# Performance work log

Hardware: AMD Instinct MI355X
Metric: run time of the kernel (lower is better)

## Reference

```python
import jax, jax.numpy as jnp
import numpy as np

K = 5  # hard-coded neighbor count in get_graph_feature


def _graph_feature(x):
    # x: (B, C, N) -> (B, 2C, N, K)
    xt = jnp.swapaxes(x, 1, 2)                      # (B, N, C)
    sq = jnp.sum(xt * xt, axis=-1)                  # (B, N)
    inner = jnp.einsum('bnc,bmc->bnm', xt, xt)      # (B, N, N)
    pdist = 2.0 * inner - sq[:, :, None] - sq[:, None, :]  # -||xi-xj||^2
    idx = jax.lax.top_k(pdist, K)[1]                # (B, N, K) nearest (incl self)
    nbr = jax.vmap(lambda f, i: f[i])(xt, idx)      # (B, N, K, C) gather
    ctr = jnp.broadcast_to(xt[:, :, None, :], nbr.shape)
    feat = jnp.concatenate([nbr, ctr], axis=-1)     # (B, N, K, 2C)
    return jnp.transpose(feat, (0, 3, 1, 2))        # (B, 2C, N, K)


def _conv1x1(w, x):
    # w: (Cout, Cin), x: (B, Cin, N, K)
    return jnp.einsum('oc,bcnk->bonk', w, x)


def setup_inputs() -> dict:
    key = jax.random.key(0)
    ks = jax.random.split(key, 6)
    B, N = 4, 8192
    x = jax.random.normal(ks[0], (B, 3, N), dtype=jnp.float32)

    def xavier(k, cout, cin):
        std = (2.0 / (cin + cout)) ** 0.5
        return std * jax.random.normal(k, (cout, cin), dtype=jnp.float32)

    return {
        'x': x,
        'w1': xavier(ks[1], 64, 6),
        'w2': xavier(ks[2], 64, 64),
        'w3': xavier(ks[3], 128, 64),
        'w4': xavier(ks[4], 256, 128),
        'w5': xavier(ks[5], 512, 512),
    }


def reference(x, w1, w2, w3, w4, w5):
    B, _, N = x.shape
    h = _graph_feature(x)                           # (B, 6, N, K)
    h = jax.nn.relu(_conv1x1(w1, h))
    x1 = jnp.max(h, axis=-1, keepdims=True)         # (B, 64, N, 1)
    h = jax.nn.relu(_conv1x1(w2, h))
    x2 = jnp.max(h, axis=-1, keepdims=True)         # (B, 64, N, 1)
    h = jax.nn.relu(_conv1x1(w3, h))
    x3 = jnp.max(h, axis=-1, keepdims=True)         # (B, 128, N, 1)
    h = jax.nn.relu(_conv1x1(w4, h))
    x4 = jnp.max(h, axis=-1, keepdims=True)         # (B, 256, N, 1)
    cat = jnp.concatenate([x1, x2, x3, x4], axis=1) # (B, 512, N, 1)
    out = jax.nn.relu(_conv1x1(w5, cat))            # (B, 512, N, 1)
    return out.reshape(B, -1, N)
```

## Files before the change

### kernel.cpp

```cpp
#include <hip/hip_runtime.h>
#include <cstdint>

#define BATCH 4
#define NPTS  8192
#define KNN   5
#define CAPQ  176

typedef short bf16x8 __attribute__((ext_vector_type(8)));
typedef float f32x4  __attribute__((ext_vector_type(4)));
#define MFMA16(a, b, c) __builtin_amdgcn_mfma_f32_16x16x32_bf16((a), (b), (c), 0, 0, 0)

__device__ __forceinline__ unsigned short f2bf(float x) {
    unsigned u = __float_as_uint(x);
    unsigned r = u + 0x7fffu + ((u >> 16) & 1u);
    return (unsigned short)(r >> 16);
}
__device__ __forceinline__ float bf2f(unsigned short h) {
    return __uint_as_float(((unsigned)h) << 16);
}
__device__ __forceinline__ void gload16(const void* g, void* l) {
    __builtin_amdgcn_global_load_lds(
        (const __attribute__((address_space(1))) unsigned int*)g,
        (__attribute__((address_space(3))) unsigned int*)l, 16, 0, 0);
}

__global__ __launch_bounds__(256) void wsplit_kernel(
        const float* __restrict__ w3, const float* __restrict__ w4,
        const float* __restrict__ w5, const float* __restrict__ x,
        unsigned short* __restrict__ w3H, unsigned short* __restrict__ w3L,
        unsigned short* __restrict__ w4H, unsigned short* __restrict__ w4L,
        unsigned short* __restrict__ w5H, unsigned short* __restrict__ w5L,
        float* __restrict__ c2) {
    const int i = blockIdx.x * 256 + threadIdx.x;
    if (i >= 303104) {
        const int pt = i - 303104;
        const int b = pt >> 13, n = pt & 8191;
        const float* xb = x + (size_t)b * 3 * NPTS;
        const float cx = xb[n], cy = xb[NPTS + n], cz = xb[2 * NPTS + n];
        c2[pt] = fmaf(cz, cz, fmaf(cy, cy, cx * cx));
        return;
    }
    const float* src; unsigned short *dh, *dl; int off;
    if (i < 8192)       { src = w3; dh = w3H; dl = w3L; off = i; }
    else if (i < 40960) { src = w4; dh = w4H; dl = w4L; off = i - 8192; }
    else                { src = w5; dh = w5H; dl = w5L; off = i - 40960; }
    const float v = src[off];
    const unsigned short hi = f2bf(v);
    dh[off] = hi;
    dl[off] = f2bf(v - bf2f(hi));
}

__global__ __launch_bounds__(1024, 8) void knn_kernel(const float* __restrict__ x,
                                                      const float* __restrict__ c2,
                                                      int* __restrict__ idx_out) {
    __shared__ __align__(16) char sbuf[32768];
    __shared__ __align__(16) char buf2[45056];
    __shared__ float  thrQ[64];
    __shared__ int    qcnt[64];

    float* thrA = (float*)buf2;
    int*   qidx = (int*)buf2;

    const int t = threadIdx.x;
    const int lane = t & 63;
    const int s = t >> 6;
    const int b = blockIdx.x >> 7;
    const int q0 = (blockIdx.x & 127) * 64;
    const int qg = q0 + lane;
    const float* xb = x + (size_t)b * 3 * NPTS;

    float4* stw = ((float4*)sbuf) + s * 128;
    double* qd  = (double*)sbuf;

    const float nqx = -2.0f * xb[qg];
    const float nqy = -2.0f * xb[NPTS + qg];
    const float nqz = -2.0f * xb[2 * NPTS + qg];

    if (t < 64) qcnt[t] = 0;

    const float2* gx = (const float2*)xb;
    const float2* gy = (const float2*)(xb + NPTS);
    const float2* gz = (const float2*)(xb + 2 * NPTS);
    const float2* gc = (const float2*)(c2 + b * NPTS);
    const int f2base = s * 256;

    float s0 = 3e38f, s1 = 3e38f, s2 = 3e38f, s3 = 3e38f, s4 = 3e38f;
    {
        float2 xv = gx[f2base + lane], yv = gy[f2base + lane];
        float2 zv = gz[f2base + lane], cv = gc[f2base + lane];
        for (int ch = 0; ch < 4; ++ch) {
            stw[0 * 64 + lane] = make_float4(xv.x, yv.x, zv.x, cv.x);
            stw[1 * 64 + lane] = make_float4(xv.y, yv.y, zv.y, cv.y);
            if (ch < 3) {
                const int f2 = f2base + (ch + 1) * 64 + lane;
                xv = gx[f2]; yv = gy[f2]; zv = gz[f2]; cv = gc[f2];
            }
            for (int u4 = 0; u4 < 32; ++u4) {
                float4 cd[4];
                #pragma unroll
                for (int j = 0; j < 4; ++j) cd[j] = stw[u4 * 4 + j];
                float d[4];
                #pragma unroll
                for (int j = 0; j < 4; ++j)
                    d[j] = fmaf(cd[j].x, nqx,
                           fmaf(cd[j].y, nqy, fmaf(cd[j].z, nqz, cd[j].w)));
                const float m0 = fminf(d[0], d[1]);
                const float m1 = fminf(d[2], d[3]);
                s4 = __builtin_amdgcn_fmed3f(s3, m0, s4);
                s3 = __builtin_amdgcn_fmed3f(s2, m0, s3);
                s2 = __builtin_amdgcn_fmed3f(s1, m0, s2);
                s1 = __builtin_amdgcn_fmed3f(s0, m0, s1);
                s0 = fminf(s0, m0);
                s4 = __builtin_amdgcn_fmed3f(s3, m1, s4);
                s3 = __builtin_amdgcn_fmed3f(s2, m1, s3);
                s2 = __builtin_amdgcn_fmed3f(s1, m1, s2);
                s1 = __builtin_amdgcn_fmed3f(s0, m1, s1);
                s0 = fminf(s0, m1);
            }
        }
    }
    thrA[s * 64 + lane] = s4;
    __syncthreads();
    if (t < 64) {
        float m = thrA[t];
        #pragma unroll
        for (int ww = 1; ww < 16; ++ww) m = fminf(m, thrA[ww * 64 + t]);
        thrQ[t] = m + 4e-4f;
    }
    __syncthreads();

    const float thrq = thrQ[lane];
    {
        float2 xv = gx[f2base + lane], yv = gy[f2base + lane];
        float2 zv = gz[f2base + lane], cv = gc[f2base + lane];
        for (int ch = 0; ch < 4; ++ch) {
            const int cb = s * 512 + ch * 128;
            stw[0 * 64 + lane] = make_float4(xv.x, yv.x, zv.x, cv.x);
            stw[1 * 64 + lane] = make_float4(xv.y, yv.y, zv.y, cv.y);
            if (ch < 3) {
                const int f2 = f2base + (ch + 1) * 64 + lane;
                xv = gx[f2]; yv = gy[f2]; zv = gz[f2]; cv = gc[f2];
            }
            for (int u4 = 0; u4 < 32; ++u4) {
                float4 cd[4];
                #pragma unroll
                for (int j = 0; j < 4; ++j) cd[j] = stw[u4 * 4 + j];
                float d[4];
                #pragma unroll
                for (int j = 0; j < 4; ++j)
                    d[j] = fmaf(cd[j].x, nqx,
                           fmaf(cd[j].y, nqy, fmaf(cd[j].z, nqz, cd[j].w)));
                const float dmin = fminf(fminf(d[0], d[1]), fminf(d[2], d[3]));
                if (dmin < thrq) {
                    #pragma unroll
                    for (int j = 0; j < 4; ++j) {
                        if (d[j] < thrq) {
                            const int slot = atomicAdd(&qcnt[lane], 1);
                            const int u = u4 * 4 + j;
                            const int gid = cb + 2 * (u & 63) + (u >> 6);
                            if (slot < CAPQ) qidx[lane * CAPQ + slot] = gid;
                        }
                    }
                }
            }
        }
    }

    const int qll = t >> 6;
    const int jt = t & 63;
    for (int ph = 0; ph < 4; ++ph) {
        __syncthreads();
        const int ql = ph * 16 + qll;
        const int cnt = min(qcnt[ql], CAPQ);
        const double Qx = (double)xb[q0 + ql];
        const double Qy = (double)xb[NPTS + q0 + ql];
        const double Qz = (double)xb[2 * NPTS + q0 + ql];
        for (int j = jt; j < cnt; j += 64) {
            const int ci = qidx[ql * CAPQ + j];
            const double ddx = Qx - (double)xb[ci];
            const double ddy = Qy - (double)xb[NPTS + ci];
            const double ddz = Qz - (double)xb[2 * NPTS + ci];
            qd[qll * CAPQ + j] = ddx * ddx + ddy * ddy + ddz * ddz;
        }
        __syncthreads();
        for (int j = jt; j < cnt; j += 64) {
            const double dj = qd[qll * CAPQ + j];
            const int    ij = qidx[ql * CAPQ + j];
            int rank = 0;
            for (int k = 0; k < cnt; ++k) {
                const double dk = qd[qll * CAPQ + k];
                const int    ik = qidx[ql * CAPQ + k];
                rank += (dk < dj) || (dk == dj && ik < ij);
            }
            if (rank < KNN)
                idx_out[((size_t)b * NPTS + q0 + ql) * KNN + rank] = ij;
        }
    }
}

__global__ __launch_bounds__(256) void mlp12_kernel(const float* __restrict__ x,
                                                    const int* __restrict__ idx,
                                                    const float* __restrict__ w1,
                                                    const float* __restrict__ w2,
                                                    unsigned short* __restrict__ h2HL,
                                                    unsigned short* __restrict__ catH,
                                                    unsigned short* __restrict__ catL) {
    __shared__ float w1s[64 * 6];
    __shared__ float w2s[64 * 68];
    __shared__ float fbuf[80][6];
    __shared__ float h1s[80 * 68];
    __shared__ float h2s[80 * 68];
    const int t = threadIdx.x;
    const int pbase = blockIdx.x * 16;

    for (int i = t; i < 384; i += 256) w1s[i] = w1[i];
    for (int i = t; i < 4096; i += 256) {
        int c = i >> 6, q = i & 63;
        w2s[c * 68 + q] = w2[i];
    }
    if (t < 80) {
        const int pt = pbase + t / 5;
        const int b = pt >> 13;
        const int n = pt & 8191;
        const int k = t % 5;
        const int j = idx[(size_t)pt * KNN + k];
        const float* xb = x + (size_t)b * 3 * NPTS;
        fbuf[t][0] = xb[j];
        fbuf[t][1] = xb[NPTS + j];
        fbuf[t][2] = xb[2 * NPTS + j];
        fbuf[t][3] = xb[n];
        fbuf[t][4] = xb[NPTS + n];
        fbuf[t][5] = xb[2 * NPTS + n];
    }
    __syncthreads();

    for (int o = t; o < 5120; o += 256) {
        const int r = o >> 6, c = o & 63;
        float acc = 0.f;
        #pragma unroll
        for (int q = 0; q < 6; ++q) acc = fmaf(w1s[c * 6 + q], fbuf[r][q], acc);
        h1s[r * 68 + c] = fmaxf(acc, 0.f);
    }
    __syncthreads();

    for (int o = t; o < 1024; o += 256) {
        const int p = o >> 6, c = o & 63;
        float m = h1s[(p * 5) * 68 + c];
        #pragma unroll
        for (int k = 1; k < 5; ++k) m = fmaxf(m, h1s[(p * 5 + k) * 68 + c]);
        const unsigned short hi = f2bf(m);
        const size_t co = (size_t)(pbase + p) * 512 + c;
        catH[co] = hi;
        catL[co] = f2bf(m - bf2f(hi));
    }

    for (int tile = t; tile < 320; tile += 256) {
        const int r0 = (tile % 20) * 4;
        const int c0 = (tile / 20) * 4;
        float acc[4][4] = {};
        for (int q = 0; q < 64; q += 4) {
            float4 a[4], w[4];
            #pragma unroll
            for (int i = 0; i < 4; ++i) a[i] = *(const float4*)&h1s[(r0 + i) * 68 + q];
            #pragma unroll
            for (int j = 0; j < 4; ++j) w[j] = *(const float4*)&w2s[(c0 + j) * 68 + q];
            #pragma unroll
            for (int i = 0; i < 4; ++i)
                #pragma unroll
                for (int j = 0; j < 4; ++j) {
                    acc[i][j] = fmaf(a[i].x, w[j].x, acc[i][j]);
                    acc[i][j] = fmaf(a[i].y, w[j].y, acc[i][j]);
                    acc[i][j] = fmaf(a[i].z, w[j].z, acc[i][j]);
                    acc[i][j] = fmaf(a[i].w, w[j].w, acc[i][j]);
                }
        }
        #pragma unroll
        for (int i = 0; i < 4; ++i)
            #pragma unroll
            for (int j = 0; j < 4; ++j)
                h2s[(r0 + i) * 68 + c0 + j] = fmaxf(acc[i][j], 0.f);
    }
    __syncthreads();

    for (int o = t; o < 1024; o += 256) {
        const int p = o >> 6, c = o & 63;
        float m = h2s[(p * 5) * 68 + c];
        #pragma unroll
        for (int k = 1; k < 5; ++k) m = fmaxf(m, h2s[(p * 5 + k) * 68 + c]);
        const unsigned short hi = f2bf(m);
        const size_t co = (size_t)(pbase + p) * 512 + 64 + c;
        catH[co] = hi;
        catL[co] = f2bf(m - bf2f(hi));
    }
    for (int o = t; o < 5120; o += 256) {
        const int r = o >> 6, c = o & 63;
        const float v = h2s[r * 68 + c];
        const unsigned short hi = f2bf(v);
        const size_t rowb = (size_t)(pbase * 5 + r) * 128;
        h2HL[rowb + c]      = hi;
        h2HL[rowb + 64 + c] = f2bf(v - bf2f(hi));
    }
}

__global__ __launch_bounds__(256) void mlp3_kernel(
        const unsigned short* __restrict__ h2HL,
        const unsigned short* __restrict__ w3H, const unsigned short* __restrict__ w3L,
        unsigned short* __restrict__ h3H, unsigned short* __restrict__ h3L,
        unsigned short* __restrict__ catH, unsigned short* __restrict__ catL) {
    __shared__ __align__(16) char smem[59904];
    unsigned short* aH = (unsigned short*)smem;
    unsigned short* aL = aH + 80 * 72;
    unsigned short* bH = (unsigned short*)(smem + 23040);
    unsigned short* bL = (unsigned short*)(smem + 41472);

    const int t = threadIdx.x;
    const int R0 = blockIdx.x * 80;
    const int P0 = blockIdx.x * 16;

    for (int c = t; c < 1280; c += 256) {
        const int row = c >> 4, seg = c & 15;
        const uint4 v = *(const uint4*)(h2HL + (size_t)(R0 + row) * 128 + seg * 8);
        *(uint4*)((seg < 8 ? aH : aL) + row * 72 + (seg & 7) * 8) = v;
    }
    for (int c = t; c < 1024; c += 256) {
        const int row = c >> 3, seg = c & 7;
        *(uint4*)(bH + row * 72 + seg * 8) =
            *(const uint4*)(w3H + row * 64 + seg * 8);
    }
    for (int c = t; c < 1024; c += 256) {
        const int row = c >> 3, seg = c & 7;
        *(uint4*)(bL + row * 72 + seg * 8) =
            *(const uint4*)(w3L + row * 64 + seg * 8);
    }
    __syncthreads();

    const int w = t >> 6, lane = t & 63;
    const int q = lane >> 4, l16 = lane & 15;
    const int n0 = w * 32;

    f32x4 acc[5][2];
    #pragma unroll
    for (int mt = 0; mt < 5; ++mt)
        #pragma unroll
        for (int nt = 0; nt < 2; ++nt)
            acc[mt][nt] = (f32x4){0.f, 0.f, 0.f, 0.f};

    #pragma unroll
    for (int kt = 0; kt < 2; ++kt) {
        const int k0 = kt * 32 + q * 8;
        bf16x8 bh[2], bl[2];
        #pragma unroll
        for (int nt = 0; nt < 2; ++nt) {
            bh[nt] = *(const bf16x8*)(bH + (n0 + nt * 16 + l16) * 72 + k0);
            bl[nt] = *(const bf16x8*)(bL + (n0 + nt * 16 + l16) * 72 + k0);
        }
        #pragma unroll
        for (int mt = 0; mt < 5; ++mt) {
            const bf16x8 ah = *(const bf16x8*)(aH + (mt * 16 + l16) * 72 + k0);
            const bf16x8 al = *(const bf16x8*)(aL + (mt * 16 + l16) * 72 + k0);
            #pragma unroll
            for (int nt = 0; nt < 2; ++nt) {
                acc[mt][nt] = MFMA16(ah, bh[nt], acc[mt][nt]);
                acc[mt][nt] = MFMA16(ah, bl[nt], acc[mt][nt]);
                acc[mt][nt] = MFMA16(al, bh[nt], acc[mt][nt]);
            }
        }
    }

    __syncthreads();
    float* Dbuf = (float*)smem;
    #pragma unroll
    for (int mt = 0; mt < 5; ++mt)
        #pragma unroll
        for (int nt = 0; nt < 2; ++nt)
            #pragma unroll
            for (int r = 0; r < 4; ++r)
                Dbuf[(mt * 16 + q * 4 + r) * 132 + n0 + nt * 16 + l16] =
                    fmaxf(acc[mt][nt][r], 0.f);
    __syncthreads();

    {
        const int col = t & 127;
        const int p0 = (t >> 7) * 8;
        #pragma unroll
        for (int p = 0; p < 8; ++p) {
            const int pp = p0 + p;
            float mx = 0.f;
            #pragma unroll
            for (int k = 0; k < 5; ++k) {
                const int row = pp * 5 + k;
                const float v = Dbuf[row * 132 + col];
                const unsigned short hi = f2bf(v);
                const unsigned short lo = f2bf(v - bf2f(hi));
                const size_t off = (size_t)(R0 + row) * 128 + col;
                h3H[off] = hi;
                h3L[off] = lo;
                mx = fmaxf(mx, bf2f(hi) + bf2f(lo));
            }
            const unsigned short mh = f2bf(mx);
            const size_t co = (size_t)(P0 + pp) * 512 + 128 + col;
            catH[co] = mh;
            catL[co] = f2bf(mx - bf2f(mh));
        }
    }
}

__global__ __launch_bounds__(256) void mlp4_kernel(
        const unsigned short* __restrict__ h3H, const unsigned short* __restrict__ h3L,
        const unsigned short* __restrict__ w4H, const unsigned short* __restrict__ w4L,
        unsigned short* __restrict__ catH, unsigned short* __restrict__ catL) {
    __shared__ __align__(16) char smem[64000];
    unsigned short* aH = (unsigned short*)smem;
    unsigned short* aL = aH + 80 * 136;
    unsigned short* bH = (unsigned short*)(smem + 43520);
    unsigned short* bL = (unsigned short*)(smem + 53760);

    const int t = threadIdx.x;
    const int R0 = blockIdx.x * 80;
    const int P0 = blockIdx.x * 16;
    const int ny = blockIdx.y;

    for (int c = t; c < 1280; c += 256) {
        const int row = c >> 4, seg = c & 15;
        *(uint4*)(aH + row * 136 + seg * 8) =
            *(const uint4*)(h3H + (size_t)(R0 + row) * 128 + seg * 8);
    }
    for (int c = t; c < 1280; c += 256) {
        const int row = c >> 4, seg = c & 15;
        *(uint4*)(aL + row * 136 + seg * 8) =
            *(const uint4*)(h3L + (size_t)(R0 + row) * 128 + seg * 8);
    }

    const int w = t >> 6, lane = t & 63;
    const int q = lane >> 4, l16 = lane & 15;
    const int n0 = w * 32;

    f32x4 acc[5][2];
    #pragma unroll
    for (int mt = 0; mt < 5; ++mt)
        #pragma unroll
        for (int nt = 0; nt < 2; ++nt)
            acc[mt][nt] = (f32x4){0.f, 0.f, 0.f, 0.f};

    for (int ks = 0; ks < 4; ++ks) {
        __syncthreads();
        #pragma unroll
        for (int i = 0; i < 2; ++i) {
            const int c = t + i * 256;
            const int row = c >> 2, seg = c & 3;
            *(uint4*)(bH + row * 40 + seg * 8) =
                *(const uint4*)(w4H + (size_t)(ny * 128 + row) * 128 + ks * 32 + seg * 8);
        }
        #pragma unroll
        for (int i = 0; i < 2; ++i) {
            const int c = t + i * 256;
            const int row = c >> 2, seg = c & 3;
            *(uint4*)(bL + row * 40 + seg * 8) =
                *(const uint4*)(w4L + (size_t)(ny * 128 + row) * 128 + ks * 32 + seg * 8);
        }
        __syncthreads();

        const int k0 = ks * 32 + q * 8;
        const int kb = q * 8;
        bf16x8 bh[2], bl[2];
        #pragma unroll
        for (int nt = 0; nt < 2; ++nt) {
            bh[nt] = *(const bf16x8*)(bH + (n0 + nt * 16 + l16) * 40 + kb);
            bl[nt] = *(const bf16x8*)(bL + (n0 + nt * 16 + l16) * 40 + kb);
        }
        #pragma unroll
        for (int mt = 0; mt < 5; ++mt) {
            const bf16x8 ah = *(const bf16x8*)(aH + (mt * 16 + l16) * 136 + k0);
            const bf16x8 al = *(const bf16x8*)(aL + (mt * 16 + l16) * 136 + k0);
            #pragma unroll
            for (int nt = 0; nt < 2; ++nt) {
                acc[mt][nt] = MFMA16(ah, bh[nt], acc[mt][nt]);
                acc[mt][nt] = MFMA16(ah, bl[nt], acc[mt][nt]);
                acc[mt][nt] = MFMA16(al, bh[nt], acc[mt][nt]);
            }
        }
    }

    __syncthreads();
    float* Dbuf = (float*)smem;
    #pragma unroll
    for (int mt = 0; mt < 5; ++mt)
        #pragma unroll
        for (int nt = 0; nt < 2; ++nt)
            #pragma unroll
            for (int r = 0; r < 4; ++r)
                Dbuf[(mt * 16 + q * 4 + r) * 132 + n0 + nt * 16 + l16] =
                    fmaxf(acc[mt][nt][r], 0.f);
    __syncthreads();

    {
        const int col = t & 127;
        const int p0 = (t >> 7) * 8;
        const int cout = 256 + ny * 128 + col;
        #pragma unroll
        for (int p = 0; p < 8; ++p) {
            const int pp = p0 + p;
            float mx = 0.f;
            #pragma unroll
            for (int k = 0; k < 5; ++k)
                mx = fmaxf(mx, Dbuf[(pp * 5 + k) * 132 + col]);
            const unsigned short mh = f2bf(mx);
            const size_t co = (size_t)(P0 + pp) * 512 + cout;
            catH[co] = mh;
            catL[co] = f2bf(mx - bf2f(mh));
        }
    }
}

__global__ __launch_bounds__(256) void gemm512_kernel(
        const unsigned short* __restrict__ catH, const unsigned short* __restrict__ catL,
        const unsigned short* __restrict__ w5H, const unsigned short* __restrict__ w5L,
        float* __restrict__ out) {
    __shared__ __align__(16) char smem[32768];
    unsigned short* aH = (unsigned short*)smem;
    unsigned short* aL = aH + 128 * 32;
    unsigned short* bH = (unsigned short*)(smem + 16384);
    unsigned short* bL = (unsigned short*)(smem + 24576);

    const int t = threadIdx.x;
    const int m0 = blockIdx.x * 128;
    const int n0blk = blockIdx.y * 128;

    const int w = t >> 6, lane = t & 63;
    const int q = lane >> 4, l16 = lane & 15;
    const int m_off = (w >> 1) * 64;
    const int n_off = (w & 1) * 64;

    const int srow = w * 32 + (lane >> 2);
    const int sseg = lane & 3;
    const size_t ar0 = (size_t)(m0 + srow) * 512 + sseg * 8;
    const size_t ar1 = ar0 + 16 * 512;
    const size_t br0 = (size_t)(n0blk + srow) * 512 + sseg * 8;
    const size_t br1 = br0 + 16 * 512;
    const int ld0 = w * 1024;

    f32x4 acc[4][4];
    #pragma unroll
    for (int mt = 0; mt < 4; ++mt)
        #pragma unroll
        for (int nt = 0; nt < 4; ++nt)
            acc[mt][nt] = (f32x4){0.f, 0.f, 0.f, 0.f};

    for (int kc = 0; kc < 512; kc += 32) {
        __syncthreads();
        gload16(catH + ar0 + kc, aH + ld0);
        gload16(catH + ar1 + kc, aH + ld0 + 512);
        gload16(catL + ar0 + kc, aL + ld0);
        gload16(catL + ar1 + kc, aL + ld0 + 512);
        gload16(w5H + br0 + kc, bH + ld0);
        gload16(w5H + br1 + kc, bH + ld0 + 512);
        gload16(w5L + br0 + kc, bL + ld0);
        gload16(w5L + br1 + kc, bL + ld0 + 512);
        __syncthreads();

        const int k0 = q * 8;
        bf16x8 bh[4], bl[4];
        #pragma unroll
        for (int nt = 0; nt < 4; ++nt) {
            bh[nt] = *(const bf16x8*)(bH + (n_off + nt * 16 + l16) * 32 + k0);
            bl[nt] = *(const bf16x8*)(bL + (n_off + nt * 16 + l16) * 32 + k0);
        }
        #pragma unroll
        for (int mt = 0; mt < 4; ++mt) {
            const bf16x8 ah = *(const bf16x8*)(aH + (m_off + mt * 16 + l16) * 32 + k0);
            const bf16x8 al = *(const bf16x8*)(aL + (m_off + mt * 16 + l16) * 32 + k0);
            #pragma unroll
            for (int nt = 0; nt < 4; ++nt) {
                acc[mt][nt] = MFMA16(ah, bh[nt], acc[mt][nt]);
                acc[mt][nt] = MFMA16(ah, bl[nt], acc[mt][nt]);
                acc[mt][nt] = MFMA16(al, bh[nt], acc[mt][nt]);
            }
        }
    }

    float* bandbuf = (float*)smem;
    for (int b8 = 0; b8 < 8; ++b8) {
        __syncthreads();
        if ((w >> 1) == (b8 >> 2)) {
            const int mt = b8 & 3;
            #pragma unroll
            for (int nt = 0; nt < 4; ++nt)
                #pragma unroll
                for (int r = 0; r < 4; ++r)
                    bandbuf[(q * 4 + r) * 132 + n_off + nt * 16 + l16] =
                        fmaxf(acc[mt][nt][r], 0.f);
        }
        __syncthreads();
        const int col = t >> 1;
        const int ph = (t & 1) * 8;
        const int P = m0 + b8 * 16 + ph;
        const int bb = P >> 13, nn = P & 8191;
        const int cout = n0blk + col;
        float tmp[8];
        #pragma unroll
        for (int j = 0; j < 8; ++j) tmp[j] = bandbuf[(ph + j) * 132 + col];
        float* op = &out[((size_t)bb * 512 + cout) * NPTS + nn];
        *(float4*)op       = make_float4(tmp[0], tmp[1], tmp[2], tmp[3]);
        *(float4*)(op + 4) = make_float4(tmp[4], tmp[5], tmp[6], tmp[7]);
    }
}

extern "C" void kernel_launch(void* const* d_in, const int* in_sizes, int n_in,
                              void* d_out, int out_size, void* d_ws, size_t ws_size,
                              hipStream_t stream) {
    (void)in_sizes; (void)n_in; (void)out_size; (void)ws_size;
    const float* x  = (const float*)d_in[0];
    const float* w1 = (const float*)d_in[1];
    const float* w2 = (const float*)d_in[2];
    const float* w3 = (const float*)d_in[3];
    const float* w4 = (const float*)d_in[4];
    const float* w5 = (const float*)d_in[5];
    float* out = (float*)d_out;

    char* ws = (char*)d_ws;
    unsigned short* w3H = (unsigned short*)(ws + 0);
    unsigned short* w3L = (unsigned short*)(ws + 16384);
    unsigned short* w4H = (unsigned short*)(ws + 32768);
    unsigned short* w4L = (unsigned short*)(ws + 98304);
    unsigned short* w5H = (unsigned short*)(ws + 163840);
    unsigned short* w5L = (unsigned short*)(ws + 688128);
    int*            idx = (int*)(ws + 1212416);
    unsigned short* catH = (unsigned short*)(ws + 2097152);
    unsigned short* catL = (unsigned short*)(ws + 35651584);
    unsigned short* h3H  = (unsigned short*)(ws + 69206016);
    float*          c2d  = (float*)(ws + 111149056);
    unsigned short* h2HL = (unsigned short*)d_out;
    unsigned short* h3L  = (unsigned short*)d_out;

    wsplit_kernel<<<dim3(1312), dim3(256), 0, stream>>>(w3, w4, w5, x,
                                                        w3H, w3L, w4H, w4L, w5H, w5L,
                                                        c2d);
    knn_kernel<<<dim3(BATCH * NPTS / 64), dim3(1024), 0, stream>>>(x, c2d, idx);
    mlp12_kernel<<<dim3(BATCH * NPTS / 16), dim3(256), 0, stream>>>(x, idx, w1, w2,
                                                                    h2HL, catH, catL);
    mlp3_kernel<<<dim3(BATCH * NPTS * KNN / 80), dim3(256), 0, stream>>>(
        h2HL, w3H, w3L, h3H, h3L, catH, catL);
    mlp4_kernel<<<dim3(BATCH * NPTS * KNN / 80, 2), dim3(256), 0, stream>>>(
        h3H, h3L, w4H, w4L, catH, catL);
    gemm512_kernel<<<dim3(BATCH * NPTS / 128, 4), dim3(256), 0, stream>>>(
        catH, catL, w5H, w5L, out);
}
```

Measured before the change: 408.1 us.

## Fuse mlp3 and mlp4 kernels, keeping layer-3 activations in shared memory

```diff
diff --git a/kernel.cpp b/kernel.cpp
--- a/kernel.cpp
+++ b/kernel.cpp
@@ -302,16 +302,16 @@
     }
 }
 
-__global__ __launch_bounds__(256) void mlp3_kernel(
+__global__ __launch_bounds__(256) void mlp34_kernel(
         const unsigned short* __restrict__ h2HL,
         const unsigned short* __restrict__ w3H, const unsigned short* __restrict__ w3L,
-        unsigned short* __restrict__ h3H, unsigned short* __restrict__ h3L,
+        const unsigned short* __restrict__ w4H, const unsigned short* __restrict__ w4L,
         unsigned short* __restrict__ catH, unsigned short* __restrict__ catL) {
-    __shared__ __align__(16) char smem[59904];
-    unsigned short* aH = (unsigned short*)smem;
-    unsigned short* aL = aH + 80 * 72;
-    unsigned short* bH = (unsigned short*)(smem + 23040);
-    unsigned short* bL = (unsigned short*)(smem + 41472);
+    __shared__ __align__(16) char smem[64000];
+    unsigned short* aH  = (unsigned short*)smem;
+    unsigned short* aL  = aH + 80 * 72;
+    unsigned short* bH3 = (unsigned short*)(smem + 23040);
+    unsigned short* bL3 = (unsigned short*)(smem + 41472);
 
     const int t = threadIdx.x;
     const int R0 = blockIdx.x * 80;
@@ -324,12 +324,12 @@
     }
     for (int c = t; c < 1024; c += 256) {
         const int row = c >> 3, seg = c & 7;
-        *(uint4*)(bH + row * 72 + seg * 8) =
+        *(uint4*)(bH3 + row * 72 + seg * 8) =
             *(const uint4*)(w3H + row * 64 + seg * 8);
     }
     for (int c = t; c < 1024; c += 256) {
         const int row = c >> 3, seg = c & 7;
-        *(uint4*)(bL + row * 72 + seg * 8) =
+        *(uint4*)(bL3 + row * 72 + seg * 8) =
             *(const uint4*)(w3L + row * 64 + seg * 8);
     }
     __syncthreads();
@@ -338,12 +338,12 @@
     const int q = lane >> 4, l16 = lane & 15;
     const int n0 = w * 32;
 
-    f32x4 acc[5][2];
+    f32x4 acc3[5][2];
     #pragma unroll
     for (int mt = 0; mt < 5; ++mt)
         #pragma unroll
         for (int nt = 0; nt < 2; ++nt)
-            acc[mt][nt] = (f32x4){0.f, 0.f, 0.f, 0.f};
+            acc3[mt][nt] = (f32x4){0.f, 0.f, 0.f, 0.f};
 
     #pragma unroll
     for (int kt = 0; kt < 2; ++kt) {
@@ -351,8 +351,8 @@
         bf16x8 bh[2], bl[2];
         #pragma unroll
         for (int nt = 0; nt < 2; ++nt) {
-            bh[nt] = *(const bf16x8*)(bH + (n0 + nt * 16 + l16) * 72 + k0);
-            bl[nt] = *(const bf16x8*)(bL + (n0 + nt * 16 + l16) * 72 + k0);
+            bh[nt] = *(const bf16x8*)(bH3 + (n0 + nt * 16 + l16) * 72 + k0);
+            bl[nt] = *(const bf16x8*)(bL3 + (n0 + nt * 16 + l16) * 72 + k0);
         }
         #pragma unroll
         for (int mt = 0; mt < 5; ++mt) {
@@ -360,25 +360,30 @@
             const bf16x8 al = *(const bf16x8*)(aL + (mt * 16 + l16) * 72 + k0);
             #pragma unroll
             for (int nt = 0; nt < 2; ++nt) {
-                acc[mt][nt] = MFMA16(ah, bh[nt], acc[mt][nt]);
-                acc[mt][nt] = MFMA16(ah, bl[nt], acc[mt][nt]);
-                acc[mt][nt] = MFMA16(al, bh[nt], acc[mt][nt]);
-            }
-        }
-    }
-
-    __syncthreads();
-    float* Dbuf = (float*)smem;
+                acc3[mt][nt] = MFMA16(ah, bh[nt], acc3[mt][nt]);
+                acc3[mt][nt] = MFMA16(ah, bl[nt], acc3[mt][nt]);
+                acc3[mt][nt] = MFMA16(al, bh[nt], acc3[mt][nt]);
+            }
+        }
+    }
+
+    __syncthreads();
+    unsigned short* a2H = (unsigned short*)smem;
+    unsigned short* a2L = a2H + 80 * 136;
     #pragma unroll
     for (int mt = 0; mt < 5; ++mt)
         #pragma unroll
         for (int nt = 0; nt < 2; ++nt)
             #pragma unroll
-            for (int r = 0; r < 4; ++r)
-                Dbuf[(mt * 16 + q * 4 + r) * 132 + n0 + nt * 16 + l16] =
-                    fmaxf(acc[mt][nt][r], 0.f);
-    __syncthreads();
-
+            for (int r = 0; r < 4; ++r) {
+                const int row = mt * 16 + q * 4 + r;
+                const int col = n0 + nt * 16 + l16;
+                const float v = fmaxf(acc3[mt][nt][r], 0.f);
+                const unsigned short hi = f2bf(v);
+                a2H[row * 136 + col] = hi;
+                a2L[row * 136 + col] = f2bf(v - bf2f(hi));
+            }
+    __syncthreads();
     {
         const int col = t & 127;
         const int p0 = (t >> 7) * 8;
@@ -389,13 +394,9 @@
             #pragma unroll
             for (int k = 0; k < 5; ++k) {
                 const int row = pp * 5 + k;
-                const float v = Dbuf[row * 132 + col];
-                const unsigned short hi = f2bf(v);
-                const unsigned short lo = f2bf(v - bf2f(hi));
-                const size_t off = (size_t)(R0 + row) * 128 + col;
-                h3H[off] = hi;
-                h3L[off] = lo;
-                mx = fmaxf(mx, bf2f(hi) + bf2f(lo));
+                const float v = bf2f(a2H[row * 136 + col]) +
+                                bf2f(a2L[row * 136 + col]);
+                mx = fmaxf(mx, v);
             }
             const unsigned short mh = f2bf(mx);
             const size_t co = (size_t)(P0 + pp) * 512 + 128 + col;
@@ -403,111 +404,89 @@
             catL[co] = f2bf(mx - bf2f(mh));
         }
     }
-}
-
-__global__ __launch_bounds__(256) void mlp4_kernel(
-        const unsigned short* __restrict__ h3H, const unsigned short* __restrict__ h3L,
-        const unsigned short* __restrict__ w4H, const unsigned short* __restrict__ w4L,
-        unsigned short* __restrict__ catH, unsigned short* __restrict__ catL) {
-    __shared__ __align__(16) char smem[64000];
-    unsigned short* aH = (unsigned short*)smem;
-    unsigned short* aL = aH + 80 * 136;
-    unsigned short* bH = (unsigned short*)(smem + 43520);
-    unsigned short* bL = (unsigned short*)(smem + 53760);
-
-    const int t = threadIdx.x;
-    const int R0 = blockIdx.x * 80;
-    const int P0 = blockIdx.x * 16;
-    const int ny = blockIdx.y;
-
-    for (int c = t; c < 1280; c += 256) {
-        const int row = c >> 4, seg = c & 15;
-        *(uint4*)(aH + row * 136 + seg * 8) =
-            *(const uint4*)(h3H + (size_t)(R0 + row) * 128 + seg * 8);
-    }
-    for (int c = t; c < 1280; c += 256) {
-        const int row = c >> 4, seg = c & 15;
-        *(uint4*)(aL + row * 136 + seg * 8) =
-            *(const uint4*)(h3L + (size_t)(R0 + row) * 128 + seg * 8);
-    }
-
-    const int w = t >> 6, lane = t & 63;
-    const int q = lane >> 4, l16 = lane & 15;
-    const int n0 = w * 32;
-
-    f32x4 acc[5][2];
+
+    unsigned short* bH4 = (unsigned short*)(smem + 43520);
+    unsigned short* bL4 = (unsigned short*)(smem + 53760);
+    f32x4 acc4[2][5][2];
     #pragma unroll
-    for (int mt = 0; mt < 5; ++mt)
-        #pragma unroll
-        for (int nt = 0; nt < 2; ++nt)
-            acc[mt][nt] = (f32x4){0.f, 0.f, 0.f, 0.f};
-
-    for (int ks = 0; ks < 4; ++ks) {
-        __syncthreads();
-        #pragma unroll
-        for (int i = 0; i < 2; ++i) {
-            const int c = t + i * 256;
-            const int row = c >> 2, seg = c & 3;
-            *(uint4*)(bH + row * 40 + seg * 8) =
-                *(const uint4*)(w4H + (size_t)(ny * 128 + row) * 128 + ks * 32 + seg * 8);
-        }
-        #pragma unroll
-        for (int i = 0; i < 2; ++i) {
-            const int c = t + i * 256;
-            const int row = c >> 2, seg = c & 3;
-            *(uint4*)(bL + row * 40 + seg * 8) =
-                *(const uint4*)(w4L + (size_t)(ny * 128 + row) * 128 + ks * 32 + seg * 8);
-        }
-        __syncthreads();
-
-        const int k0 = ks * 32 + q * 8;
-        const int kb = q * 8;
-        bf16x8 bh[2], bl[2];
-        #pragma unroll
-        for (int nt = 0; nt < 2; ++nt) {
-            bh[nt] = *(const bf16x8*)(bH + (n0 + nt * 16 + l16) * 40 + kb);
-            bl[nt] = *(const bf16x8*)(bL + (n0 + nt * 16 + l16) * 40 + kb);
-        }
-        #pragma unroll
-        for (int mt = 0; mt < 5; ++mt) {
-            const bf16x8 ah = *(const bf16x8*)(aH + (mt * 16 + l16) * 136 + k0);
-            const bf16x8 al = *(const bf16x8*)(aL + (mt * 16 + l16) * 136 + k0);
+    for (int ny = 0; ny < 2; ++ny)
+        #pragma unroll
+        for (int mt = 0; mt < 5; ++mt)
+            #pragma unroll
+            for (int nt = 0; nt < 2; ++nt)
+                acc4[ny][mt][nt] = (f32x4){0.f, 0.f, 0.f, 0.f};
+
+    #pragma unroll
+    for (int ny = 0; ny < 2; ++ny) {
+        for (int ks = 0; ks < 4; ++ks) {
+            __syncthreads();
+            #pragma unroll
+            for (int i = 0; i < 2; ++i) {
+                const int c = t + i * 256;
+                const int row = c >> 2, seg = c & 3;
+                *(uint4*)(bH4 + row * 40 + seg * 8) =
+                    *(const uint4*)(w4H + (size_t)(ny * 128 + row) * 128 + ks * 32 + seg * 8);
+            }
+            #pragma unroll
+            for (int i = 0; i < 2; ++i) {
+                const int c = t + i * 256;
+                const int row = c >> 2, seg = c & 3;
+                *(uint4*)(bL4 + row * 40 + seg * 8) =
+                    *(const uint4*)(w4L + (size_t)(ny * 128 + row) * 128 + ks * 32 + seg * 8);
+            }
+            __syncthreads();
+
+            const int k0 = ks * 32 + q * 8;
+            const int kb = q * 8;
+            bf16x8 bh[2], bl[2];
             #pragma unroll
             for (int nt = 0; nt < 2; ++nt) {
-                acc[mt][nt] = MFMA16(ah, bh[nt], acc[mt][nt]);
-                acc[mt][nt] = MFMA16(ah, bl[nt], acc[mt][nt]);
-                acc[mt][nt] = MFMA16(al, bh[nt], acc[mt][nt]);
-            }
-        }
-    }
-
-    __syncthreads();
+                bh[nt] = *(const bf16x8*)(bH4 + (n0 + nt * 16 + l16) * 40 + kb);
+                bl[nt] = *(const bf16x8*)(bL4 + (n0 + nt * 16 + l16) * 40 + kb);
+            }
+            #pragma unroll
+            for (int mt = 0; mt < 5; ++mt) {
+                const bf16x8 ah = *(const bf16x8*)(a2H + (mt * 16 + l16) * 136 + k0);
+                const bf16x8 al = *(const bf16x8*)(a2L + (mt * 16 + l16) * 136 + k0);
+                #pragma unroll
+                for (int nt = 0; nt < 2; ++nt) {
+                    acc4[ny][mt][nt] = MFMA16(ah, bh[nt], acc4[ny][mt][nt]);
+                    acc4[ny][mt][nt] = MFMA16(ah, bl[nt], acc4[ny][mt][nt]);
+                    acc4[ny][mt][nt] = MFMA16(al, bh[nt], acc4[ny][mt][nt]);
+                }
+            }
+        }
+    }
+
     float* Dbuf = (float*)smem;
     #pragma unroll
-    for (int mt = 0; mt < 5; ++mt)
-        #pragma unroll
-        for (int nt = 0; nt < 2; ++nt)
-            #pragma unroll
-            for (int r = 0; r < 4; ++r)
-                Dbuf[(mt * 16 + q * 4 + r) * 132 + n0 + nt * 16 + l16] =
-                    fmaxf(acc[mt][nt][r], 0.f);
-    __syncthreads();
-
-    {
-        const int col = t & 127;
-        const int p0 = (t >> 7) * 8;
-        const int cout = 256 + ny * 128 + col;
-        #pragma unroll
-        for (int p = 0; p < 8; ++p) {
-            const int pp = p0 + p;
-            float mx = 0.f;
-            #pragma unroll
-            for (int k = 0; k < 5; ++k)
-                mx = fmaxf(mx, Dbuf[(pp * 5 + k) * 132 + col]);
-            const unsigned short mh = f2bf(mx);
-            const size_t co = (size_t)(P0 + pp) * 512 + cout;
-            catH[co] = mh;
-            catL[co] = f2bf(mx - bf2f(mh));
+    for (int ny = 0; ny < 2; ++ny) {
+        __syncthreads();
+        #pragma unroll
+        for (int mt = 0; mt < 5; ++mt)
+            #pragma unroll
+            for (int nt = 0; nt < 2; ++nt)
+                #pragma unroll
+                for (int r = 0; r < 4; ++r)
+                    Dbuf[(mt * 16 + q * 4 + r) * 132 + n0 + nt * 16 + l16] =
+                        fmaxf(acc4[ny][mt][nt][r], 0.f);
+        __syncthreads();
+        {
+            const int col = t & 127;
+            const int p0 = (t >> 7) * 8;
+            const int cout = 256 + ny * 128 + col;
+            #pragma unroll
+            for (int p = 0; p < 8; ++p) {
+                const int pp = p0 + p;
+                float mx = 0.f;
+                #pragma unroll
+                for (int k = 0; k < 5; ++k)
+                    mx = fmaxf(mx, Dbuf[(pp * 5 + k) * 132 + col]);
+                const unsigned short mh = f2bf(mx);
+                const size_t co = (size_t)(P0 + pp) * 512 + cout;
+                catH[co] = mh;
+                catL[co] = f2bf(mx - bf2f(mh));
+            }
         }
     }
 }
@@ -627,10 +606,8 @@
     int*            idx = (int*)(ws + 1212416);
     unsigned short* catH = (unsigned short*)(ws + 2097152);
     unsigned short* catL = (unsigned short*)(ws + 35651584);
-    unsigned short* h3H  = (unsigned short*)(ws + 69206016);
-    float*          c2d  = (float*)(ws + 111149056);
+    float*          c2d  = (float*)(ws + 69206016);
     unsigned short* h2HL = (unsigned short*)d_out;
-    unsigned short* h3L  = (unsigned short*)d_out;
 
     wsplit_kernel<<<dim3(1312), dim3(256), 0, stream>>>(w3, w4, w5, x,
                                                         w3H, w3L, w4H, w4L, w5H, w5L,
@@ -638,10 +615,8 @@
     knn_kernel<<<dim3(BATCH * NPTS / 64), dim3(1024), 0, stream>>>(x, c2d, idx);
     mlp12_kernel<<<dim3(BATCH * NPTS / 16), dim3(256), 0, stream>>>(x, idx, w1, w2,
                                                                     h2HL, catH, catL);
-    mlp3_kernel<<<dim3(BATCH * NPTS * KNN / 80), dim3(256), 0, stream>>>(
-        h2HL, w3H, w3L, h3H, h3L, catH, catL);
-    mlp4_kernel<<<dim3(BATCH * NPTS * KNN / 80, 2), dim3(256), 0, stream>>>(
-        h3H, h3L, w4H, w4L, catH, catL);
+    mlp34_kernel<<<dim3(BATCH * NPTS * KNN / 80), dim3(256), 0, stream>>>(
+        h2HL, w3H, w3L, w4H, w4L, catH, catL);
     gemm512_kernel<<<dim3(BATCH * NPTS / 128, 4), dim3(256), 0, stream>>>(
         catH, catL, w5H, w5L, out);
 }
```

New measurement: 375.1 us (median of 2 runs). 8.1% less time.
